# Optimization experiments

Measured on AMD Instinct MI355X. Metric: run time of the kernel, lower is better.

Reference implementation:

```python
import jax, jax.numpy as jnp
import numpy as np

LUT_SIZE = 4096
TWO_PI = 2.0 * np.pi


def _lut_tables():
    idx = jnp.arange(LUT_SIZE, dtype=jnp.float32)
    ang = idx * (TWO_PI / LUT_SIZE)
    return jnp.sin(ang), jnp.cos(ang)


def lut_sin_cos(theta):
    """4096-entry LUT sin/cos with linear interpolation, period 2*pi."""
    sin_t, cos_t = _lut_tables()
    fidx = theta * (LUT_SIZE / TWO_PI)
    i0f = jnp.floor(fidx)
    w = fidx - i0f  # interpolation weight in [0,1)
    i0 = jnp.mod(i0f.astype(jnp.int32), LUT_SIZE)
    i1 = jnp.mod(i0 + 1, LUT_SIZE)
    s = sin_t[i0] * (1.0 - w) + sin_t[i1] * w
    c = cos_t[i0] * (1.0 - w) + cos_t[i1] * w
    return s, c


def setup_inputs() -> dict:
    key = jax.random.key(0)
    ks = jax.random.split(key, 9)
    B_, D, N = 32, 1024, 2048
    return {
        "x_real": jax.random.normal(ks[0], (B_, D), jnp.float32),
        "x_imag": jax.random.normal(ks[1], (B_, D), jnp.float32),
        "t": jax.random.uniform(ks[2], (B_,), jnp.float32),
        "input_proj_w": jax.random.normal(ks[3], (D, 2 * D), jnp.float32) * (1.0 / np.sqrt(2 * D)),
        "input_proj_b": jnp.zeros((D,), jnp.float32),
        "W": jax.random.normal(ks[4], (N, D), jnp.float32) * 0.02,
        "B": jnp.zeros((N, D), jnp.float32),
        "out_real_w": jax.random.normal(ks[5], (D, N), jnp.float32) * (1.0 / np.sqrt(N)),
        "out_imag_w": jax.random.normal(ks[6], (D, N), jnp.float32) * (1.0 / np.sqrt(N)),
    }


def reference(x_real, x_imag, t, input_proj_w, input_proj_b, W, B, out_real_w, out_imag_w):
    # input projection on concatenated real/imag: (batch, d_model)
    x_combined = jnp.concatenate([x_real, x_imag], axis=-1)
    x_collapsed = x_combined @ input_proj_w.T + input_proj_b
    # broadcast: (batch, 1, d) / (n, d) + (n, d) + (batch, 1, 1)
    wavelength = 1.0 + jnp.abs(W)
    theta = x_collapsed[:, None, :] / wavelength + B + t[:, None, None]
    sin_theta, cos_theta = lut_sin_cos(theta)
    cos_sum = cos_theta.sum(axis=-1)  # (batch, n)
    sin_sum = sin_theta.sum(axis=-1)
    out_real = cos_sum @ out_real_w.T
    out_imag = sin_sum @ out_imag_w.T
    return jax.nn.silu(out_real), jax.nn.silu(out_imag)
```

## Files before the change

### kernel.cpp

```cpp
#include <hip/hip_runtime.h>
#include <math.h>

#define D_MODEL 1024
#define N_RES   2048
#define BATCH   32
constexpr float INV_2PI = 0.15915494309189535f;

#define WS_XC 0
#define WS_CS (BATCH * D_MODEL)
#define WS_SS (WS_CS + BATCH * N_RES)

template <int V>
__device__ __forceinline__ void bstage(float* acc, int lane, int m) {
  const bool hi = (lane & m) != 0;
#pragma unroll
  for (int v = 0; v < V / 2; ++v) {
    float send = hi ? acc[v] : acc[v + V / 2];
    float keep = hi ? acc[v + V / 2] : acc[v];
    acc[v] = keep + __shfl_xor(send, m, 64);
  }
}

__device__ __forceinline__ float silu(float v) { return v / (1.f + __expf(-v)); }

__global__ __launch_bounds__(512) void kA(const float* __restrict__ xr,
                                          const float* __restrict__ xi,
                                          const float* __restrict__ ipw,
                                          const float* __restrict__ bias,
                                          float* __restrict__ xc) {
  const int tid  = threadIdx.x;
  const int lane = tid & 63;
  const int wave = tid >> 6;
  const int d0 = blockIdx.x * 4;
  const int b0 = wave * 4;

  const float4* xr4  = (const float4*)xr;
  const float4* xi4  = (const float4*)xi;
  const float4* ipw4 = (const float4*)ipw;

  float acc[16];
#pragma unroll
  for (int v = 0; v < 16; ++v) acc[v] = 0.f;

#pragma unroll 2
  for (int i = 0; i < 4; ++i) {
    const int j = lane + 64 * i;
    float4 w4[4], x4[4];
#pragma unroll
    for (int d = 0; d < 4; ++d) w4[d] = ipw4[(d0 + d) * 512 + j];
#pragma unroll
    for (int b = 0; b < 4; ++b) x4[b] = xr4[(b0 + b) * 256 + j];
#pragma unroll
    for (int b = 0; b < 4; ++b)
#pragma unroll
      for (int d = 0; d < 4; ++d)
        acc[(b << 2) | d] += x4[b].x * w4[d].x + x4[b].y * w4[d].y +
                             x4[b].z * w4[d].z + x4[b].w * w4[d].w;
  }
#pragma unroll 2
  for (int i = 0; i < 4; ++i) {
    const int j = lane + 64 * i;
    float4 w4[4], x4[4];
#pragma unroll
    for (int d = 0; d < 4; ++d) w4[d] = ipw4[(d0 + d) * 512 + 256 + j];
#pragma unroll
    for (int b = 0; b < 4; ++b) x4[b] = xi4[(b0 + b) * 256 + j];
#pragma unroll
    for (int b = 0; b < 4; ++b)
#pragma unroll
      for (int d = 0; d < 4; ++d)
        acc[(b << 2) | d] += x4[b].x * w4[d].x + x4[b].y * w4[d].y +
                             x4[b].z * w4[d].z + x4[b].w * w4[d].w;
  }

  bstage<16>(acc, lane, 32);
  bstage<8>(acc, lane, 16);
  bstage<4>(acc, lane, 8);
  bstage<2>(acc, lane, 4);
  float r = acc[0];
  r += __shfl_xor(r, 2, 64);
  r += __shfl_xor(r, 1, 64);
  if ((lane & 3) == 0) {
    const int b = (lane >> 4) & 3;
    const int d = (lane >> 2) & 3;
    xc[(size_t)(b0 + b) * D_MODEL + d0 + d] = r + bias[d0 + d];
  }
}

__device__ __forceinline__ void sc1(float xv, float av, float cv, float t2,
                                    float& ca, float& sa) {
  float r = __builtin_fmaf(xv, av, cv + t2);
  float fr;
  asm("v_fract_f32 %0, %1" : "=v"(fr) : "v"(r));
  sa += __builtin_amdgcn_sinf(fr);
  ca += __builtin_amdgcn_cosf(fr);
}

__global__ __launch_bounds__(256) void kB(const float* __restrict__ xc,
                                          const float* __restrict__ W,
                                          const float* __restrict__ Bm,
                                          const float* __restrict__ t,
                                          float* __restrict__ cos_sum,
                                          float* __restrict__ sin_sum) {
  __shared__ float a_s[2][D_MODEL];
  __shared__ float c_s[2][D_MODEL];
  const int n0  = blockIdx.x * 2;
  const int tid = threadIdx.x;

#pragma unroll
  for (int rr = 0; rr < 2; ++rr) {
    float4 w4 = ((const float4*)(W + (size_t)(n0 + rr) * D_MODEL))[tid];
    float4 b4 = ((const float4*)(Bm + (size_t)(n0 + rr) * D_MODEL))[tid];
    float4 a4, c4;
    a4.x = INV_2PI / (1.f + fabsf(w4.x));
    a4.y = INV_2PI / (1.f + fabsf(w4.y));
    a4.z = INV_2PI / (1.f + fabsf(w4.z));
    a4.w = INV_2PI / (1.f + fabsf(w4.w));
    c4.x = b4.x * INV_2PI;
    c4.y = b4.y * INV_2PI;
    c4.z = b4.z * INV_2PI;
    c4.w = b4.w * INV_2PI;
    ((float4*)a_s[rr])[tid] = a4;
    ((float4*)c_s[rr])[tid] = c4;
  }
  __syncthreads();

  const int lane = tid & 63;
  const int wave = tid >> 6;
  const int b0 = wave * 8;
  const float4* as4 = (const float4*)a_s;
  const float4* cs4 = (const float4*)c_s;

#pragma unroll 1
  for (int bb = 0; bb < 8; ++bb) {
    const int b = b0 + bb;
    const float t2 = t[b] * INV_2PI;
    const float4* x4p = (const float4*)(xc + (size_t)b * D_MODEL);
    float acc[4] = {0.f, 0.f, 0.f, 0.f};
#pragma unroll
    for (int i = 0; i < 4; ++i) {
      const int j = lane + 64 * i;
      float4 x4 = x4p[j];
#pragma unroll
      for (int rr = 0; rr < 2; ++rr) {
        float4 a4 = as4[rr * 256 + j];
        float4 c4 = cs4[rr * 256 + j];
        sc1(x4.x, a4.x, c4.x, t2, acc[rr], acc[2 + rr]);
        sc1(x4.y, a4.y, c4.y, t2, acc[rr], acc[2 + rr]);
        sc1(x4.z, a4.z, c4.z, t2, acc[rr], acc[2 + rr]);
        sc1(x4.w, a4.w, c4.w, t2, acc[rr], acc[2 + rr]);
      }
    }
    bstage<4>(acc, lane, 32);
    bstage<2>(acc, lane, 16);
    float v0 = acc[0];
    v0 += __shfl_xor(v0, 8, 64);
    v0 += __shfl_xor(v0, 4, 64);
    v0 += __shfl_xor(v0, 2, 64);
    v0 += __shfl_xor(v0, 1, 64);
    if ((lane & 15) == 0) {
      const int sc = (lane >> 5) & 1;
      const int rr = (lane >> 4) & 1;
      float* dst = sc ? sin_sum : cos_sum;
      dst[(size_t)b * N_RES + n0 + rr] = v0;
    }
  }
}

__global__ __launch_bounds__(512) void kC(const float* __restrict__ cos_sum,
                                          const float* __restrict__ sin_sum,
                                          const float* __restrict__ orw,
                                          const float* __restrict__ oiw,
                                          float* __restrict__ out) {
  const int tid  = threadIdx.x;
  const int lane = tid & 63;
  const int wave = tid >> 6;
  const int d0 = blockIdx.x * 4;
  const int b0 = wave * 4;

  const float4* cs4p = (const float4*)cos_sum;
  const float4* sn4p = (const float4*)sin_sum;
  const float4* orw4 = (const float4*)orw;
  const float4* oiw4 = (const float4*)oiw;

  float acc[32];
#pragma unroll
  for (int v = 0; v < 32; ++v) acc[v] = 0.f;

#pragma unroll 2
  for (int i = 0; i < 8; ++i) {
    const int j = lane + 64 * i;
    float4 cs[4], sn[4];
#pragma unroll
    for (int b = 0; b < 4; ++b) {
      cs[b] = cs4p[(b0 + b) * 512 + j];
      sn[b] = sn4p[(b0 + b) * 512 + j];
    }
#pragma unroll
    for (int d = 0; d < 4; ++d) {
      float4 wr = orw4[(d0 + d) * 512 + j];
      float4 wi = oiw4[(d0 + d) * 512 + j];
#pragma unroll
      for (int b = 0; b < 4; ++b) {
        acc[(b << 2) | d] += cs[b].x * wr.x + cs[b].y * wr.y +
                             cs[b].z * wr.z + cs[b].w * wr.w;
        acc[16 | (b << 2) | d] += sn[b].x * wi.x + sn[b].y * wi.y +
                                  sn[b].z * wi.z + sn[b].w * wi.w;
      }
    }
  }

  bstage<32>(acc, lane, 32);
  bstage<16>(acc, lane, 16);
  bstage<8>(acc, lane, 8);
  bstage<4>(acc, lane, 4);
  bstage<2>(acc, lane, 2);
  float v = acc[0] + __shfl_xor(acc[0], 1, 64);
  if ((lane & 1) == 0) {
    const int comp = (lane >> 5) & 1;
    const int b = (lane >> 3) & 3;
    const int d = (lane >> 1) & 3;
    const size_t o = (size_t)(b0 + b) * D_MODEL + d0 + d;
    out[(size_t)comp * (BATCH * D_MODEL) + o] = silu(v);
  }
}

extern "C" void kernel_launch(void* const* d_in, const int* in_sizes, int n_in,
                              void* d_out, int out_size, void* d_ws, size_t ws_size,
                              hipStream_t stream) {
  const float* xr   = (const float*)d_in[0];
  const float* xi   = (const float*)d_in[1];
  const float* t    = (const float*)d_in[2];
  const float* ipw  = (const float*)d_in[3];
  const float* bias = (const float*)d_in[4];
  const float* W    = (const float*)d_in[5];
  const float* Bm   = (const float*)d_in[6];
  const float* orw  = (const float*)d_in[7];
  const float* oiw  = (const float*)d_in[8];
  float* out = (float*)d_out;

  float* ws      = (float*)d_ws;
  float* xc      = ws + WS_XC;
  float* cos_sum = ws + WS_CS;
  float* sin_sum = ws + WS_SS;

  kA<<<256, 512, 0, stream>>>(xr, xi, ipw, bias, xc);
  kB<<<N_RES / 2, 256, 0, stream>>>(xc, W, Bm, t, cos_sum, sin_sum);
  kC<<<256, 512, 0, stream>>>(cos_sum, sin_sum, orw, oiw, out);
}
```

Measured before the change: 138.5 us.

## Factor time phase out of sin/cos sums, bf16 intermediates, wider kB tiles

The per-batch time offset is pulled out of the inner trig loop by angle-addition: the sums are computed without t and then rotated by cos(t) and sin(t) once per output. This also drops v_fract on the reduced argument, relying on the hardware sin/cos handling the unreduced range. kB now processes 4 residues per block with 512 threads. The cos/sin sums are stored as bf16, which halves the traffic that kC reads. The risks are lower precision in the bf16 intermediates and reduced accuracy of hardware sin/cos on larger arguments.

```diff
diff --git a/kernel.cpp b/kernel.cpp
--- a/kernel.cpp
+++ b/kernel.cpp
@@ -8,7 +8,9 @@
 
 #define WS_XC 0
 #define WS_CS (BATCH * D_MODEL)
-#define WS_SS (WS_CS + BATCH * N_RES)
+
+typedef unsigned int uint;
+typedef unsigned short ushort;
 
 template <int V>
 __device__ __forceinline__ void bstage(float* acc, int lane, int m) {
@@ -22,6 +24,17 @@
 }
 
 __device__ __forceinline__ float silu(float v) { return v / (1.f + __expf(-v)); }
+
+__device__ __forceinline__ ushort f2bf(float f) {
+  uint u = __builtin_bit_cast(uint, f);
+  u += 0x7fffu + ((u >> 16) & 1u);
+  return (ushort)(u >> 16);
+}
+
+__device__ __forceinline__ void unpk(uint u, float& lo, float& hi) {
+  lo = __builtin_bit_cast(float, u << 16);
+  hi = __builtin_bit_cast(float, u & 0xffff0000u);
+}
 
 __global__ __launch_bounds__(512) void kA(const float* __restrict__ xr,
                                           const float* __restrict__ xi,
@@ -87,30 +100,25 @@
   }
 }
 
-__device__ __forceinline__ void sc1(float xv, float av, float cv, float t2,
-                                    float& ca, float& sa) {
-  float r = __builtin_fmaf(xv, av, cv + t2);
-  float fr;
-  asm("v_fract_f32 %0, %1" : "=v"(fr) : "v"(r));
-  sa += __builtin_amdgcn_sinf(fr);
-  ca += __builtin_amdgcn_cosf(fr);
-}
-
-__global__ __launch_bounds__(256) void kB(const float* __restrict__ xc,
+#define NT 4
+__global__ __launch_bounds__(512) void kB(const float* __restrict__ xc,
                                           const float* __restrict__ W,
                                           const float* __restrict__ Bm,
                                           const float* __restrict__ t,
-                                          float* __restrict__ cos_sum,
-                                          float* __restrict__ sin_sum) {
-  __shared__ float a_s[2][D_MODEL];
-  __shared__ float c_s[2][D_MODEL];
-  const int n0  = blockIdx.x * 2;
+                                          ushort* __restrict__ cos_sum,
+                                          ushort* __restrict__ sin_sum) {
+  __shared__ float a_s[NT][D_MODEL];
+  __shared__ float c_s[NT][D_MODEL];
+  const int n0  = blockIdx.x * NT;
   const int tid = threadIdx.x;
 
 #pragma unroll
-  for (int rr = 0; rr < 2; ++rr) {
-    float4 w4 = ((const float4*)(W + (size_t)(n0 + rr) * D_MODEL))[tid];
-    float4 b4 = ((const float4*)(Bm + (size_t)(n0 + rr) * D_MODEL))[tid];
+  for (int k = 0; k < 2; ++k) {
+    const int idx = tid + k * 512;
+    const int rr = idx >> 8;
+    const int j  = idx & 255;
+    float4 w4 = ((const float4*)(W + (size_t)(n0 + rr) * D_MODEL))[j];
+    float4 b4 = ((const float4*)(Bm + (size_t)(n0 + rr) * D_MODEL))[j];
     float4 a4, c4;
     a4.x = INV_2PI / (1.f + fabsf(w4.x));
     a4.y = INV_2PI / (1.f + fabsf(w4.y));
@@ -120,55 +128,71 @@
     c4.y = b4.y * INV_2PI;
     c4.z = b4.z * INV_2PI;
     c4.w = b4.w * INV_2PI;
-    ((float4*)a_s[rr])[tid] = a4;
-    ((float4*)c_s[rr])[tid] = c4;
+    ((float4*)a_s[rr])[j] = a4;
+    ((float4*)c_s[rr])[j] = c4;
   }
   __syncthreads();
 
   const int lane = tid & 63;
   const int wave = tid >> 6;
-  const int b0 = wave * 8;
-  const float4* as4 = (const float4*)a_s;
-  const float4* cs4 = (const float4*)c_s;
+  const int b0 = wave * 4;
 
 #pragma unroll 1
-  for (int bb = 0; bb < 8; ++bb) {
+  for (int bb = 0; bb < 4; ++bb) {
     const int b = b0 + bb;
     const float t2 = t[b] * INV_2PI;
+    const float tc = __builtin_amdgcn_cosf(t2);
+    const float ts = __builtin_amdgcn_sinf(t2);
     const float4* x4p = (const float4*)(xc + (size_t)b * D_MODEL);
-    float acc[4] = {0.f, 0.f, 0.f, 0.f};
+    float acc[2 * NT];
+#pragma unroll
+    for (int v = 0; v < 2 * NT; ++v) acc[v] = 0.f;
+
 #pragma unroll
     for (int i = 0; i < 4; ++i) {
       const int j = lane + 64 * i;
       float4 x4 = x4p[j];
 #pragma unroll
-      for (int rr = 0; rr < 2; ++rr) {
-        float4 a4 = as4[rr * 256 + j];
-        float4 c4 = cs4[rr * 256 + j];
-        sc1(x4.x, a4.x, c4.x, t2, acc[rr], acc[2 + rr]);
-        sc1(x4.y, a4.y, c4.y, t2, acc[rr], acc[2 + rr]);
-        sc1(x4.z, a4.z, c4.z, t2, acc[rr], acc[2 + rr]);
-        sc1(x4.w, a4.w, c4.w, t2, acc[rr], acc[2 + rr]);
+      for (int rr = 0; rr < NT; ++rr) {
+        float4 a4 = ((const float4*)a_s[rr])[j];
+        float4 c4 = ((const float4*)c_s[rr])[j];
+        float u;
+        u = __builtin_fmaf(x4.x, a4.x, c4.x);
+        acc[rr] += __builtin_amdgcn_cosf(u);
+        acc[NT + rr] += __builtin_amdgcn_sinf(u);
+        u = __builtin_fmaf(x4.y, a4.y, c4.y);
+        acc[rr] += __builtin_amdgcn_cosf(u);
+        acc[NT + rr] += __builtin_amdgcn_sinf(u);
+        u = __builtin_fmaf(x4.z, a4.z, c4.z);
+        acc[rr] += __builtin_amdgcn_cosf(u);
+        acc[NT + rr] += __builtin_amdgcn_sinf(u);
+        u = __builtin_fmaf(x4.w, a4.w, c4.w);
+        acc[rr] += __builtin_amdgcn_cosf(u);
+        acc[NT + rr] += __builtin_amdgcn_sinf(u);
       }
     }
-    bstage<4>(acc, lane, 32);
-    bstage<2>(acc, lane, 16);
+
+    bstage<8>(acc, lane, 32);
+    bstage<4>(acc, lane, 16);
+    bstage<2>(acc, lane, 8);
     float v0 = acc[0];
-    v0 += __shfl_xor(v0, 8, 64);
     v0 += __shfl_xor(v0, 4, 64);
     v0 += __shfl_xor(v0, 2, 64);
     v0 += __shfl_xor(v0, 1, 64);
-    if ((lane & 15) == 0) {
-      const int sc = (lane >> 5) & 1;
-      const int rr = (lane >> 4) & 1;
-      float* dst = sc ? sin_sum : cos_sum;
-      dst[(size_t)b * N_RES + n0 + rr] = v0;
-    }
-  }
-}
-
-__global__ __launch_bounds__(512) void kC(const float* __restrict__ cos_sum,
-                                          const float* __restrict__ sin_sum,
+    const float other = __shfl_xor(v0, 32, 64);
+    if ((lane & 7) == 0) {
+      const int sc = lane >> 5;
+      const int rr = (lane >> 3) & 3;
+      const float outv = sc ? __builtin_fmaf(tc, v0, ts * other)
+                            : __builtin_fmaf(tc, v0, -ts * other);
+      ushort* dst = sc ? sin_sum : cos_sum;
+      dst[(size_t)b * N_RES + n0 + rr] = f2bf(outv);
+    }
+  }
+}
+
+__global__ __launch_bounds__(512) void kC(const ushort* __restrict__ cos_sum,
+                                          const ushort* __restrict__ sin_sum,
                                           const float* __restrict__ orw,
                                           const float* __restrict__ oiw,
                                           float* __restrict__ out) {
@@ -178,8 +202,8 @@
   const int d0 = blockIdx.x * 4;
   const int b0 = wave * 4;
 
-  const float4* cs4p = (const float4*)cos_sum;
-  const float4* sn4p = (const float4*)sin_sum;
+  const uint4* cs4p = (const uint4*)cos_sum;
+  const uint4* sn4p = (const uint4*)sin_sum;
   const float4* orw4 = (const float4*)orw;
   const float4* oiw4 = (const float4*)oiw;
 
@@ -187,25 +211,43 @@
 #pragma unroll
   for (int v = 0; v < 32; ++v) acc[v] = 0.f;
 
-#pragma unroll 2
-  for (int i = 0; i < 8; ++i) {
+#pragma unroll 1
+  for (int i = 0; i < 4; ++i) {
     const int j = lane + 64 * i;
-    float4 cs[4], sn[4];
+    uint4 cq[4], sq[4];
 #pragma unroll
     for (int b = 0; b < 4; ++b) {
-      cs[b] = cs4p[(b0 + b) * 512 + j];
-      sn[b] = sn4p[(b0 + b) * 512 + j];
+      cq[b] = cs4p[(b0 + b) * 256 + j];
+      sq[b] = sn4p[(b0 + b) * 256 + j];
+    }
+    float ce[4][8], se[4][8];
+#pragma unroll
+    for (int b = 0; b < 4; ++b) {
+      unpk(cq[b].x, ce[b][0], ce[b][1]);
+      unpk(cq[b].y, ce[b][2], ce[b][3]);
+      unpk(cq[b].z, ce[b][4], ce[b][5]);
+      unpk(cq[b].w, ce[b][6], ce[b][7]);
+      unpk(sq[b].x, se[b][0], se[b][1]);
+      unpk(sq[b].y, se[b][2], se[b][3]);
+      unpk(sq[b].z, se[b][4], se[b][5]);
+      unpk(sq[b].w, se[b][6], se[b][7]);
     }
 #pragma unroll
     for (int d = 0; d < 4; ++d) {
-      float4 wr = orw4[(d0 + d) * 512 + j];
-      float4 wi = oiw4[(d0 + d) * 512 + j];
+      float4 wr0 = orw4[(d0 + d) * 512 + 2 * j];
+      float4 wr1 = orw4[(d0 + d) * 512 + 2 * j + 1];
+      float4 wi0 = oiw4[(d0 + d) * 512 + 2 * j];
+      float4 wi1 = oiw4[(d0 + d) * 512 + 2 * j + 1];
 #pragma unroll
       for (int b = 0; b < 4; ++b) {
-        acc[(b << 2) | d] += cs[b].x * wr.x + cs[b].y * wr.y +
-                             cs[b].z * wr.z + cs[b].w * wr.w;
-        acc[16 | (b << 2) | d] += sn[b].x * wi.x + sn[b].y * wi.y +
-                                  sn[b].z * wi.z + sn[b].w * wi.w;
+        acc[(b << 2) | d] += ce[b][0] * wr0.x + ce[b][1] * wr0.y +
+                             ce[b][2] * wr0.z + ce[b][3] * wr0.w +
+                             ce[b][4] * wr1.x + ce[b][5] * wr1.y +
+                             ce[b][6] * wr1.z + ce[b][7] * wr1.w;
+        acc[16 | (b << 2) | d] += se[b][0] * wi0.x + se[b][1] * wi0.y +
+                                  se[b][2] * wi0.z + se[b][3] * wi0.w +
+                                  se[b][4] * wi1.x + se[b][5] * wi1.y +
+                                  se[b][6] * wi1.z + se[b][7] * wi1.w;
       }
     }
   }
@@ -239,12 +281,12 @@
   const float* oiw  = (const float*)d_in[8];
   float* out = (float*)d_out;
 
-  float* ws      = (float*)d_ws;
-  float* xc      = ws + WS_XC;
-  float* cos_sum = ws + WS_CS;
-  float* sin_sum = ws + WS_SS;
+  float* ws = (float*)d_ws;
+  float* xc = ws + WS_XC;
+  ushort* cos_sum = (ushort*)(ws + WS_CS);
+  ushort* sin_sum = cos_sum + BATCH * N_RES;
 
   kA<<<256, 512, 0, stream>>>(xr, xi, ipw, bias, xc);
-  kB<<<N_RES / 2, 256, 0, stream>>>(xc, W, Bm, t, cos_sum, sin_sum);
+  kB<<<N_RES / NT, 512, 0, stream>>>(xc, W, Bm, t, cos_sum, sin_sum);
   kC<<<256, 512, 0, stream>>>(cos_sum, sin_sum, orw, oiw, out);
 }
```

Measured after the change: 133.2 us. 1.04x faster.
